# Kernel optimization log

Hardware: AMD Instinct MI355X
Metric: run time of the kernel (lower is better)

## Reference

```python
import jax, jax.numpy as jnp
from jax import lax
import numpy as np

T, N, H, C = 1000, 64, 1024, 256

def setup_inputs() -> dict:
    key = jax.random.key(0)
    k0, k1, k2, k3, k4 = jax.random.split(key, 5)
    s = 0.05
    return {
        "encoder_output": jax.random.normal(k0, (T, N, H), dtype=jnp.float32),
        "W_ih": jax.random.normal(k1, (3 * C, H), dtype=jnp.float32) * s,  # [r|z|n] input weights
        "W_hh": jax.random.normal(k2, (3 * C, C), dtype=jnp.float32) * s,
        "b_ih": jax.random.normal(k3, (3 * C,), dtype=jnp.float32) * s,
        "b_hh": jax.random.normal(k4, (3 * C,), dtype=jnp.float32) * s,
    }

def reference(encoder_output, W_ih, W_hh, b_ih, b_hh):
    # Batched input projection over all timesteps: [T,N,3C]
    xp = jnp.einsum('tnh,gh->tng', encoder_output, W_ih) + b_ih
    c = W_hh.shape[1]

    def step(h, xp_t):
        gh = h @ W_hh.T + b_hh                      # [N,3C]
        xr, xz, xn = jnp.split(xp_t, 3, axis=-1)
        hr, hz, hn = jnp.split(gh, 3, axis=-1)
        r = jax.nn.sigmoid(xr + hr)
        z = jax.nn.sigmoid(xz + hz)
        n = jnp.tanh(xn + r * hn)
        h_new = (1.0 - z) * n + z * h
        return h_new, h_new

    h0 = jnp.zeros((encoder_output.shape[1], c), dtype=encoder_output.dtype)
    _, out = lax.scan(step, h0, xp)                 # out: [T,N,C]
    return jax.nn.log_softmax(out, axis=2)
```

## Files before the change

### kernel.cpp

```cpp
#include <hip/hip_runtime.h>
#include <stdint.h>

#define T_STEPS 1000
#define NB      64
#define HDIM    1024
#define CDIM    256
#define G3      768
#define LOG2E   1.44269504088896340736f

typedef float f32x4  __attribute__((ext_vector_type(4)));
typedef short bf16x8 __attribute__((ext_vector_type(8)));
typedef int   i32x4  __attribute__((ext_vector_type(4)));

__device__ __forceinline__ float bf2f(unsigned short u) {
    union { unsigned int i; float f; } v; v.i = ((unsigned int)u) << 16; return v.f;
}
__device__ __forceinline__ unsigned short f2bf(float f) {
    union { float f; unsigned int i; } v; v.f = f;
    unsigned int r = v.i + 0x7fffu + ((v.i >> 16) & 1u);
    return (unsigned short)(r >> 16);
}

__device__ __forceinline__ int lane32_merge(int x01, int x23) {
#if __has_builtin(__builtin_amdgcn_permlane32_swap)
    auto r = __builtin_amdgcn_permlane32_swap(x01, x23, false, false);
    return r[0];
#else
    const int lane = threadIdx.x & 63;
    const int lo = __shfl(x23, lane & 31, 64);
    return (lane < 32) ? x01 : lo;
#endif
}

__global__ __launch_bounds__(256) void cvt_wih(
    const float* __restrict__ wih, unsigned short* __restrict__ wih_bf)
{
    int idx = blockIdx.x * 256 + threadIdx.x;
    wih_bf[idx] = f2bf(wih[idx]);
}

__global__ __launch_bounds__(64) void quant_whh(
    const float* __restrict__ whh, signed char* __restrict__ wq,
    float* __restrict__ dscale)
{
    const int g    = blockIdx.x;
    const int lane = threadIdx.x;
    const float4 w = *(const float4*)(whh + (size_t)g * CDIM + lane * 4);
    float m = fmaxf(fmaxf(fabsf(w.x), fabsf(w.y)), fmaxf(fabsf(w.z), fabsf(w.w)));
    #pragma unroll
    for (int s = 32; s > 0; s >>= 1) m = fmaxf(m, __shfl_xor(m, s, 64));
    const float inv = (m > 0.f) ? 127.f / m : 0.f;
    char4 q;
    q.x = (signed char)(int)rintf(w.x * inv);
    q.y = (signed char)(int)rintf(w.y * inv);
    q.z = (signed char)(int)rintf(w.z * inv);
    q.w = (signed char)(int)rintf(w.w * inv);
    *(char4*)(wq + (size_t)g * CDIM + lane * 4) = q;
    if (lane == 0) dscale[g] = m / (127.f * 127.f);
}

__global__ __launch_bounds__(256) void xproj_gemm(
    const float* __restrict__ enc,
    const unsigned short* __restrict__ wih,
    const float* __restrict__ bih,
    unsigned short* __restrict__ xp2)
{
    const int gt_base = blockIdx.x * 64;
    const int t       = blockIdx.y;
    const int tid  = threadIdx.x;
    const int w    = tid >> 6;
    const int lane = tid & 63;
    const int q    = lane >> 4, l15 = lane & 15;

    __shared__ unsigned short As[64][72];
    __shared__ unsigned short Bs[64][72];

    const f32x4 zero4 = {0.f, 0.f, 0.f, 0.f};
    f32x4 acc[4] = {zero4, zero4, zero4, zero4};

    const int arow = tid >> 4;
    const int acol = (tid & 15) * 4;
    const int brow = tid >> 3;
    const int bcol = (tid & 7) * 8;

    for (int kt = 0; kt < 16; ++kt) {
        const int k0 = kt * 64;
        __syncthreads();
        #pragma unroll
        for (int i = 0; i < 4; ++i) {
            const int r = arow + i * 16;
            const float4 av = *(const float4*)(enc + (size_t)(t * 64 + r) * HDIM + k0 + acol);
            ushort4 u;
            u.x = f2bf(av.x); u.y = f2bf(av.y); u.z = f2bf(av.z); u.w = f2bf(av.w);
            *(ushort4*)(&As[r][acol]) = u;
        }
        #pragma unroll
        for (int i = 0; i < 2; ++i) {
            const int r = brow + i * 32;
            const uint4 bv = *(const uint4*)(wih + (size_t)(gt_base + r) * HDIM + k0 + bcol);
            *(uint4*)(&Bs[r][bcol]) = bv;
        }
        __syncthreads();
        #pragma unroll
        for (int kk = 0; kk < 2; ++kk) {
            const bf16x8 a = *(const bf16x8*)(&As[16 * w + l15][kk * 32 + q * 8]);
            #pragma unroll
            for (int g = 0; g < 4; ++g) {
                const bf16x8 b = *(const bf16x8*)(&Bs[16 * g + l15][kk * 32 + q * 8]);
                acc[g] = __builtin_amdgcn_mfma_f32_16x16x32_bf16(a, b, acc[g], 0, 0, 0);
            }
        }
    }

    #pragma unroll
    for (int g = 0; g < 4; ++g) {
        const int gg = gt_base + 16 * g + l15;
        const float bias = bih[gg];
        ushort4 u;
        u.x = f2bf(acc[g][0] + bias);
        u.y = f2bf(acc[g][1] + bias);
        u.z = f2bf(acc[g][2] + bias);
        u.w = f2bf(acc[g][3] + bias);
        *(ushort4*)(xp2 + ((size_t)((t * 16 + 4 * w + q) * G3 + gg)) * 4) = u;
    }
}

__global__ void __launch_bounds__(512)
__attribute__((amdgpu_waves_per_eu(2, 2)))
gru_scan(
    const unsigned short* __restrict__ xp2,
    const signed char* __restrict__ wq,
    const float* __restrict__ dscale,
    const float* __restrict__ bhh,
    float* __restrict__ out)
{
    const int wg   = blockIdx.x;
    const int tid  = threadIdx.x;
    const int wv   = tid >> 6;
    const int lane = tid & 63;
    const int q    = lane >> 4, l15 = lane & 15;

    __shared__ __align__(16) signed char hbuf[2][16][304];

    i32x4 W[2][3][4];
    float d[2][3], bh[2][3];
    #pragma unroll
    for (int c = 0; c < 2; ++c)
        #pragma unroll
        for (int s = 0; s < 3; ++s) {
            const int g = 16 * (2 * wv + c) + 256 * s + l15;
            d[c][s]  = dscale[g];
            bh[c][s] = bhh[g];
            #pragma unroll
            for (int kk = 0; kk < 4; ++kk)
                W[c][s][kk] = *(const i32x4*)(wq + (size_t)g * CDIM + kk * 64 + q * 16);
        }
    #pragma unroll
    for (int c = 0; c < 2; ++c)
        #pragma unroll
        for (int s = 0; s < 3; ++s)
            asm volatile("" : "+v"(W[c][s][0]), "+v"(W[c][s][1]),
                              "+v"(W[c][s][2]), "+v"(W[c][s][3]));

    float h[2] = {0.f, 0.f};

    for (int i = tid; i < 2 * 16 * 304; i += 512) ((signed char*)hbuf)[i] = 0;
    __syncthreads();

    unsigned short xc[2][3];
    {
        const unsigned short* xpt = xp2 + (size_t)wg * (G3 * 4);
        #pragma unroll
        for (int c = 0; c < 2; ++c)
            #pragma unroll
            for (int s = 0; s < 3; ++s)
                xc[c][s] = xpt[(256 * s + 16 * (2 * wv + c) + l15) * 4 + q];
    }

    int pb = 0;
    for (int t = 0; t < T_STEPS; ++t) {
        const int tn = (t + 1 < T_STEPS) ? t + 1 : t;
        unsigned short xn_[2][3];
        {
            const unsigned short* xpt = xp2 + ((size_t)tn * 16 + wg) * (G3 * 4);
            #pragma unroll
            for (int c = 0; c < 2; ++c)
                #pragma unroll
                for (int s = 0; s < 3; ++s)
                    xn_[c][s] = xpt[(256 * s + 16 * (2 * wv + c) + l15) * 4 + q];
        }

        i32x4 acc[2][3];
        #pragma unroll
        for (int c = 0; c < 2; ++c)
            #pragma unroll
            for (int s = 0; s < 3; ++s) acc[c][s] = (i32x4){0, 0, 0, 0};
        #pragma unroll
        for (int kk = 0; kk < 4; ++kk) {
            const i32x4 a = *(const i32x4*)(&hbuf[pb][l15][kk * 64 + q * 16]);
            #pragma unroll
            for (int c = 0; c < 2; ++c) {
                acc[c][0] = __builtin_amdgcn_mfma_i32_16x16x64_i8(a, W[c][0][kk], acc[c][0], 0, 0, 0);
                acc[c][1] = __builtin_amdgcn_mfma_i32_16x16x64_i8(a, W[c][1][kk], acc[c][1], 0, 0, 0);
                acc[c][2] = __builtin_amdgcn_mfma_i32_16x16x64_i8(a, W[c][2][kk], acc[c][2], 0, 0, 0);
            }
        }

        float P[2][3];
        #pragma unroll
        for (int c = 0; c < 2; ++c)
            #pragma unroll
            for (int s = 0; s < 3; ++s) {
                const int r1b = __shfl(acc[c][s][1], l15, 64);
                const int r3b = __shfl(acc[c][s][3], l15, 64);
                const int x01 = (lane < 16) ? acc[c][s][0] : r1b;
                const int x23 = (lane < 16) ? acc[c][s][2] : r3b;
                P[c][s] = (float)lane32_merge(x01, x23);
            }

        float* outt = out + ((size_t)t * NB + wg * 4 + q) * CDIM;
        const int pbn = pb ^ 1;
        #pragma unroll
        for (int c = 0; c < 2; ++c) {
            const int jc = 32 * wv + 16 * c + l15;
            const float a_r = fmaf(d[c][0], P[c][0], bf2f(xc[c][0]) + bh[c][0]);
            const float rg  = __builtin_amdgcn_rcpf(
                1.f + __builtin_amdgcn_exp2f(-LOG2E * a_r));
            const float a_z = fmaf(d[c][1], P[c][1], bf2f(xc[c][1]) + bh[c][1]);
            const float ez  = __builtin_amdgcn_exp2f(-LOG2E * a_z);
            const float zi  = __builtin_amdgcn_rcpf(1.f + ez);
            const float hng = fmaf(d[c][2], P[c][2], bh[c][2]);
            const float na  = fmaf(rg, hng, bf2f(xc[c][2]));
            const float e2  = __builtin_amdgcn_exp2f(2.f * LOG2E * na);
            const float th  = 1.f - 2.f * __builtin_amdgcn_rcpf(e2 + 1.f);
            const float hv  = zi * fmaf(ez, th, h[c]);
            h[c] = hv;
            hbuf[pbn][q][jc] = (signed char)(int)rintf(hv * 127.f);
            outt[jc] = hv;
        }
        asm volatile("s_waitcnt lgkmcnt(0)\n\ts_barrier" ::: "memory");
        pb = pbn;
        #pragma unroll
        for (int c = 0; c < 2; ++c)
            #pragma unroll
            for (int s = 0; s < 3; ++s) xc[c][s] = xn_[c][s];
    }
}

__global__ __launch_bounds__(256) void logsoftmax_rows(float* __restrict__ out)
{
    const int tid  = threadIdx.x;
    const int wv   = tid >> 6, lane = tid & 63;
    const int row  = blockIdx.x * 4 + wv;
    float* p = out + (size_t)row * CDIM + lane * 4;
    float4 v = *(const float4*)p;

    float m = fmaxf(fmaxf(v.x, v.y), fmaxf(v.z, v.w));
    #pragma unroll
    for (int s = 32; s > 0; s >>= 1) m = fmaxf(m, __shfl_xor(m, s, 64));

    float sum = __builtin_amdgcn_exp2f((v.x - m) * LOG2E)
              + __builtin_amdgcn_exp2f((v.y - m) * LOG2E)
              + __builtin_amdgcn_exp2f((v.z - m) * LOG2E)
              + __builtin_amdgcn_exp2f((v.w - m) * LOG2E);
    #pragma unroll
    for (int s = 32; s > 0; s >>= 1) sum += __shfl_xor(sum, s, 64);

    const float lse = m + __builtin_amdgcn_logf(sum) * 0.69314718055994531f;
    v.x -= lse; v.y -= lse; v.z -= lse; v.w -= lse;
    *(float4*)p = v;
}

extern "C" void kernel_launch(void* const* d_in, const int* in_sizes, int n_in,
                              void* d_out, int out_size, void* d_ws, size_t ws_size,
                              hipStream_t stream)
{
    const float* enc = (const float*)d_in[0];
    const float* wih = (const float*)d_in[1];
    const float* whh = (const float*)d_in[2];
    const float* bih = (const float*)d_in[3];
    const float* bhh = (const float*)d_in[4];
    float* out = (float*)d_out;

    unsigned short* xp2    = (unsigned short*)d_ws;
    unsigned short* wih_bf = (unsigned short*)((char*)d_ws + 98304000);
    signed char*    whhq   = (signed char*)((char*)d_ws + 99876864);
    float*          dsc    = (float*)((char*)d_ws + 100073472);

    cvt_wih<<<dim3(3072), dim3(256), 0, stream>>>(wih, wih_bf);
    quant_whh<<<dim3(768), dim3(64), 0, stream>>>(whh, whhq, dsc);
    xproj_gemm<<<dim3(12, 1000), dim3(256), 0, stream>>>(enc, wih_bf, bih, xp2);
    gru_scan<<<dim3(16), dim3(512), 0, stream>>>(xp2, whhq, dsc, bhh, out);
    logsoftmax_rows<<<dim3(16000), dim3(256), 0, stream>>>(out);
}
```

Before: 1.578 ms.

## Split GRU scan over 16 waves with one column chunk each, use permlane swaps

The recurrent scan block grows from 8 to 16 waves, so each wave now owns a single 16-column chunk instead of two. This halves the per-wave MFMA and gate work on the serial critical path of each timestep. The accumulator compaction now uses permlane16/permlane32 swaps instead of shuffles plus selects. The cost is a barrier across twice as many waves every step, and higher occupancy per SIMD limits the registers available to each wave.

```diff
diff --git a/kernel.cpp b/kernel.cpp
--- a/kernel.cpp
+++ b/kernel.cpp
@@ -21,13 +21,20 @@
     return (unsigned short)(r >> 16);
 }
 
-__device__ __forceinline__ int lane32_merge(int x01, int x23) {
-#if __has_builtin(__builtin_amdgcn_permlane32_swap)
-    auto r = __builtin_amdgcn_permlane32_swap(x01, x23, false, false);
-    return r[0];
+__device__ __forceinline__ int pack4(i32x4 a) {
+#if __has_builtin(__builtin_amdgcn_permlane16_swap) && __has_builtin(__builtin_amdgcn_permlane32_swap)
+    auto y01 = __builtin_amdgcn_permlane16_swap(a[0], a[1], false, false);
+    auto y23 = __builtin_amdgcn_permlane16_swap(a[2], a[3], false, false);
+    auto p   = __builtin_amdgcn_permlane32_swap(y01[0], y23[0], false, false);
+    return p[0];
 #else
     const int lane = threadIdx.x & 63;
-    const int lo = __shfl(x23, lane & 31, 64);
+    const int l15  = lane & 15;
+    const int r1b = __shfl(a[1], l15, 64);
+    const int r3b = __shfl(a[3], l15, 64);
+    const int x01 = (lane < 16) ? a[0] : r1b;
+    const int x23 = (lane < 16) ? a[2] : r3b;
+    const int lo  = __shfl(x23, lane & 31, 64);
     return (lane < 32) ? x01 : lo;
 #endif
 }
@@ -125,8 +132,8 @@
     }
 }
 
-__global__ void __launch_bounds__(512)
-__attribute__((amdgpu_waves_per_eu(2, 2)))
+__global__ void __launch_bounds__(1024)
+__attribute__((amdgpu_waves_per_eu(4, 4)))
 gru_scan(
     const unsigned short* __restrict__ xp2,
     const signed char* __restrict__ wq,
@@ -139,111 +146,86 @@
     const int wv   = tid >> 6;
     const int lane = tid & 63;
     const int q    = lane >> 4, l15 = lane & 15;
+    const int jc   = 16 * wv + l15;
 
     __shared__ __align__(16) signed char hbuf[2][16][304];
 
-    i32x4 W[2][3][4];
-    float d[2][3], bh[2][3];
-    #pragma unroll
-    for (int c = 0; c < 2; ++c)
-        #pragma unroll
-        for (int s = 0; s < 3; ++s) {
-            const int g = 16 * (2 * wv + c) + 256 * s + l15;
-            d[c][s]  = dscale[g];
-            bh[c][s] = bhh[g];
-            #pragma unroll
-            for (int kk = 0; kk < 4; ++kk)
-                W[c][s][kk] = *(const i32x4*)(wq + (size_t)g * CDIM + kk * 64 + q * 16);
-        }
-    #pragma unroll
-    for (int c = 0; c < 2; ++c)
-        #pragma unroll
-        for (int s = 0; s < 3; ++s)
-            asm volatile("" : "+v"(W[c][s][0]), "+v"(W[c][s][1]),
-                              "+v"(W[c][s][2]), "+v"(W[c][s][3]));
-
-    float h[2] = {0.f, 0.f};
-
-    for (int i = tid; i < 2 * 16 * 304; i += 512) ((signed char*)hbuf)[i] = 0;
+    i32x4 W[3][4];
+    float d[3], bh[3];
+    #pragma unroll
+    for (int s = 0; s < 3; ++s) {
+        const int g = 256 * s + jc;
+        d[s]  = dscale[g];
+        bh[s] = bhh[g];
+        #pragma unroll
+        for (int kk = 0; kk < 4; ++kk)
+            W[s][kk] = *(const i32x4*)(wq + (size_t)g * CDIM + kk * 64 + q * 16);
+    }
+    #pragma unroll
+    for (int s = 0; s < 3; ++s)
+        asm volatile("" : "+v"(W[s][0]), "+v"(W[s][1]),
+                          "+v"(W[s][2]), "+v"(W[s][3]));
+
+    float h = 0.f;
+
+    for (int i = tid; i < 2 * 16 * 304; i += 1024) ((signed char*)hbuf)[i] = 0;
     __syncthreads();
 
-    unsigned short xc[2][3];
+    unsigned short xc[3];
     {
         const unsigned short* xpt = xp2 + (size_t)wg * (G3 * 4);
         #pragma unroll
-        for (int c = 0; c < 2; ++c)
-            #pragma unroll
-            for (int s = 0; s < 3; ++s)
-                xc[c][s] = xpt[(256 * s + 16 * (2 * wv + c) + l15) * 4 + q];
+        for (int s = 0; s < 3; ++s)
+            xc[s] = xpt[(256 * s + jc) * 4 + q];
     }
 
     int pb = 0;
     for (int t = 0; t < T_STEPS; ++t) {
         const int tn = (t + 1 < T_STEPS) ? t + 1 : t;
-        unsigned short xn_[2][3];
+        unsigned short xn_[3];
         {
             const unsigned short* xpt = xp2 + ((size_t)tn * 16 + wg) * (G3 * 4);
             #pragma unroll
-            for (int c = 0; c < 2; ++c)
-                #pragma unroll
-                for (int s = 0; s < 3; ++s)
-                    xn_[c][s] = xpt[(256 * s + 16 * (2 * wv + c) + l15) * 4 + q];
-        }
-
-        i32x4 acc[2][3];
-        #pragma unroll
-        for (int c = 0; c < 2; ++c)
-            #pragma unroll
-            for (int s = 0; s < 3; ++s) acc[c][s] = (i32x4){0, 0, 0, 0};
+            for (int s = 0; s < 3; ++s)
+                xn_[s] = xpt[(256 * s + jc) * 4 + q];
+        }
+
+        i32x4 acc[3];
+        #pragma unroll
+        for (int s = 0; s < 3; ++s) acc[s] = (i32x4){0, 0, 0, 0};
         #pragma unroll
         for (int kk = 0; kk < 4; ++kk) {
             const i32x4 a = *(const i32x4*)(&hbuf[pb][l15][kk * 64 + q * 16]);
-            #pragma unroll
-            for (int c = 0; c < 2; ++c) {
-                acc[c][0] = __builtin_amdgcn_mfma_i32_16x16x64_i8(a, W[c][0][kk], acc[c][0], 0, 0, 0);
-                acc[c][1] = __builtin_amdgcn_mfma_i32_16x16x64_i8(a, W[c][1][kk], acc[c][1], 0, 0, 0);
-                acc[c][2] = __builtin_amdgcn_mfma_i32_16x16x64_i8(a, W[c][2][kk], acc[c][2], 0, 0, 0);
-            }
-        }
-
-        float P[2][3];
-        #pragma unroll
-        for (int c = 0; c < 2; ++c)
-            #pragma unroll
-            for (int s = 0; s < 3; ++s) {
-                const int r1b = __shfl(acc[c][s][1], l15, 64);
-                const int r3b = __shfl(acc[c][s][3], l15, 64);
-                const int x01 = (lane < 16) ? acc[c][s][0] : r1b;
-                const int x23 = (lane < 16) ? acc[c][s][2] : r3b;
-                P[c][s] = (float)lane32_merge(x01, x23);
-            }
-
-        float* outt = out + ((size_t)t * NB + wg * 4 + q) * CDIM;
+            acc[0] = __builtin_amdgcn_mfma_i32_16x16x64_i8(a, W[0][kk], acc[0], 0, 0, 0);
+            acc[1] = __builtin_amdgcn_mfma_i32_16x16x64_i8(a, W[1][kk], acc[1], 0, 0, 0);
+            acc[2] = __builtin_amdgcn_mfma_i32_16x16x64_i8(a, W[2][kk], acc[2], 0, 0, 0);
+        }
+
+        float P[3];
+        #pragma unroll
+        for (int s = 0; s < 3; ++s) P[s] = (float)pack4(acc[s]);
+
         const int pbn = pb ^ 1;
-        #pragma unroll
-        for (int c = 0; c < 2; ++c) {
-            const int jc = 32 * wv + 16 * c + l15;
-            const float a_r = fmaf(d[c][0], P[c][0], bf2f(xc[c][0]) + bh[c][0]);
+        {
+            const float a_r = fmaf(d[0], P[0], bf2f(xc[0]) + bh[0]);
             const float rg  = __builtin_amdgcn_rcpf(
                 1.f + __builtin_amdgcn_exp2f(-LOG2E * a_r));
-            const float a_z = fmaf(d[c][1], P[c][1], bf2f(xc[c][1]) + bh[c][1]);
+            const float a_z = fmaf(d[1], P[1], bf2f(xc[1]) + bh[1]);
             const float ez  = __builtin_amdgcn_exp2f(-LOG2E * a_z);
             const float zi  = __builtin_amdgcn_rcpf(1.f + ez);
-            const float hng = fmaf(d[c][2], P[c][2], bh[c][2]);
-            const float na  = fmaf(rg, hng, bf2f(xc[c][2]));
+            const float hng = fmaf(d[2], P[2], bh[2]);
+            const float na  = fmaf(rg, hng, bf2f(xc[2]));
             const float e2  = __builtin_amdgcn_exp2f(2.f * LOG2E * na);
             const float th  = 1.f - 2.f * __builtin_amdgcn_rcpf(e2 + 1.f);
-            const float hv  = zi * fmaf(ez, th, h[c]);
-            h[c] = hv;
+            const float hv  = zi * fmaf(ez, th, h);
+            h = hv;
             hbuf[pbn][q][jc] = (signed char)(int)rintf(hv * 127.f);
-            outt[jc] = hv;
+            out[((size_t)t * NB + wg * 4 + q) * CDIM + jc] = hv;
         }
         asm volatile("s_waitcnt lgkmcnt(0)\n\ts_barrier" ::: "memory");
         pb = pbn;
         #pragma unroll
-        for (int c = 0; c < 2; ++c)
-            #pragma unroll
-            for (int s = 0; s < 3; ++s) xc[c][s] = xn_[c][s];
+        for (int s = 0; s < 3; ++s) xc[s] = xn_[s];
     }
 }
 
@@ -290,6 +272,6 @@
     cvt_wih<<<dim3(3072), dim3(256), 0, stream>>>(wih, wih_bf);
     quant_whh<<<dim3(768), dim3(64), 0, stream>>>(whh, whhq, dsc);
     xproj_gemm<<<dim3(12, 1000), dim3(256), 0, stream>>>(enc, wih_bf, bih, xp2);
-    gru_scan<<<dim3(16), dim3(512), 0, stream>>>(xp2, whhq, dsc, bhh, out);
+    gru_scan<<<dim3(16), dim3(1024), 0, stream>>>(xp2, whhq, dsc, bhh, out);
     logsoftmax_rows<<<dim3(16000), dim3(256), 0, stream>>>(out);
 }
```

Result: faster. 1.470 ms (-6.9%).
